# Kernel tuning notes

Hardware: AMD Instinct MI355X
Metric: run time of the kernel (lower is better)

## Reference

```python
import jax, jax.numpy as jnp
import numpy as np

VERTS = [5023, 1256, 314, 79, 20]
SPIRAL_LEN = 9
T_FRAMES = 32
LATENT = 64


def _spiral_conv(x, idx, W, b):
    # x: [B, N, C]; idx: [N, L]; gather spiral neighborhoods then linear
    B = x.shape[0]
    g = x[:, idx.reshape(-1), :].reshape(B, idx.shape[0], -1)  # [B, N, L*C]
    return g @ W.T + b


def _pool(x, rows, cols, vals, n_out):
    # sparse matmul: out[b, rows] += x[b, cols] * vals  (index_select + scatter_add)
    gathered = x[:, cols, :] * vals[None, :, None]
    return jnp.zeros((x.shape[0], n_out, x.shape[2]), x.dtype).at[:, rows, :].add(gathered)


def _lstm_dir(x, Wih, Whh, bih, bhh, reverse):
    # x: [T, B, D]; PyTorch gate order i, f, g, o
    Bz, H = x.shape[1], Whh.shape[1]
    bias = bih + bhh
    def step(carry, xt):
        h, c = carry
        g = xt @ Wih.T + h @ Whh.T + bias
        i, f, gg, o = jnp.split(g, 4, axis=-1)
        c = jax.nn.sigmoid(f) * c + jax.nn.sigmoid(i) * jnp.tanh(gg)
        h = jax.nn.sigmoid(o) * jnp.tanh(c)
        return (h, c), h
    init = (jnp.zeros((Bz, H), x.dtype), jnp.zeros((Bz, H), x.dtype))
    _, hs = jax.lax.scan(step, init, x, reverse=reverse)
    return hs


def _forward(audio_hidden, vertices, actor,
             sp_idx0, sp_idx1, sp_idx2, sp_idx3,
             d0_rows, d0_cols, d0_vals, d1_rows, d1_cols, d1_vals,
             d2_rows, d2_cols, d2_vals, d3_rows, d3_cols, d3_vals,
             u0_rows, u0_cols, u0_vals, u1_rows, u1_cols, u1_vals,
             u2_rows, u2_cols, u2_vals, u3_rows, u3_cols, u3_vals,
             enc_W0, enc_b0, enc_W1, enc_b1, enc_W2, enc_b2, enc_W3, enc_b3,
             enc_lin_W, enc_lin_b, dec_lin_W, dec_lin_b,
             dec_W0, dec_b0, dec_W1, dec_b1, dec_W2, dec_b2, dec_W3, dec_b3,
             dec_W4, dec_b4, aud_W, aud_b,
             l0_Wih, l0_Whh, l0_bih, l0_bhh, l12_Wih, l12_Whh, l12_bih, l12_bhh):
    ah = audio_hidden
    if ah.shape[1] % 2 != 0:
        ah = ah[:, :ah.shape[1] - 1]
    tv = vertices.shape[1]
    if ah.shape[1] > 2 * tv:
        ah = ah[:, :2 * tv]
    elif ah.shape[1] < 2 * tv:
        tv = ah.shape[1] // 2
    hs = ah.reshape(1, ah.shape[1] // 2, ah.shape[2] * 2)[:, :tv]  # [1, T, 1536]
    audio_emb = hs @ aud_W.T + aud_b                                # [1, T, LATENT]
    # --- mesh encoder on actor template: (spiral conv -> ELU -> down pool) x4 -> Linear ---
    sp = (sp_idx0, sp_idx1, sp_idx2, sp_idx3)
    down = ((d0_rows, d0_cols, d0_vals), (d1_rows, d1_cols, d1_vals),
            (d2_rows, d2_cols, d2_vals), (d3_rows, d3_cols, d3_vals))
    encp = ((enc_W0, enc_b0), (enc_W1, enc_b1), (enc_W2, enc_b2), (enc_W3, enc_b3))
    x = actor
    for i in range(4):
        x = jax.nn.elu(_spiral_conv(x, sp[i], *encp[i]))
        x = _pool(x, *down[i], VERTS[i + 1])
    z = x.reshape(x.shape[0], -1) @ enc_lin_W.T + enc_lin_b        # [1, LATENT]
    actor_emb = jnp.broadcast_to(z[:, None, :], audio_emb.shape)
    # --- 3-layer bidirectional LSTM ---
    h = jnp.concatenate([audio_emb, actor_emb], axis=-1).transpose(1, 0, 2)  # [T, 1, 2*LATENT]
    for layer in range(3):
        if layer == 0:
            Wih, Whh, bih, bhh = l0_Wih, l0_Whh, l0_bih, l0_bhh
        else:
            Wih, Whh, bih, bhh = l12_Wih[layer - 1], l12_Whh[layer - 1], l12_bih[layer - 1], l12_bhh[layer - 1]
        f = _lstm_dir(h, Wih[0], Whh[0], bih[0], bhh[0], False)
        r = _lstm_dir(h, Wih[1], Whh[1], bih[1], bhh[1], True)
        h = jnp.concatenate([f, r], axis=-1)
    latent = h.transpose(1, 0, 2)[0]                               # [T, LATENT]
    # --- mesh decoder, batched over all frames (replaces the python per-frame loop) ---
    up = ((u0_rows, u0_cols, u0_vals), (u1_rows, u1_cols, u1_vals),
          (u2_rows, u2_cols, u2_vals), (u3_rows, u3_cols, u3_vals))
    decp = ((dec_W0, dec_b0), (dec_W1, dec_b1), (dec_W2, dec_b2), (dec_W3, dec_b3))
    y = latent @ dec_lin_W.T + dec_lin_b                           # [T, 20*256]
    y = y.reshape(y.shape[0], VERTS[4], -1)                        # [T, 20, 256]
    for i in range(4):
        j = 3 - i
        y = _pool(y, *up[j], VERTS[j])
        y = jax.nn.elu(_spiral_conv(y, sp[j], *decp[i]))
    y = _spiral_conv(y, sp[0], dec_W4, dec_b4)                     # [T, 5023, 3]
    return y + actor                                               # broadcast residual, == vstacked preds


def setup_inputs() -> dict:
    key = jax.random.key(0)
    ks = iter(jax.random.split(key, 96))
    def nrm(shape, s=0.05):
        return jax.random.normal(next(ks), shape, jnp.float32) * s
    def rint(shape, hi):
        return jax.random.randint(next(ks), shape, 0, hi)
    inp = {}
    inp['audio_hidden'] = nrm((1, 2 * T_FRAMES, 768), 1.0)
    inp['vertices'] = nrm((1, T_FRAMES, VERTS[0], 3), 1.0)
    inp['actor'] = nrm((1, VERTS[0], 3), 1.0)
    for i in range(4):
        inp['sp_idx%d' % i] = rint((VERTS[i], SPIRAL_LEN), VERTS[i])
    for i in range(4):
        nnz = 3 * VERTS[i + 1]
        inp['d%d_rows' % i] = rint((nnz,), VERTS[i + 1])
        inp['d%d_cols' % i] = rint((nnz,), VERTS[i])
        inp['d%d_vals' % i] = jax.random.uniform(next(ks), (nnz,), jnp.float32)
    for i in range(4):
        nnz = 3 * VERTS[i]
        inp['u%d_rows' % i] = rint((nnz,), VERTS[i])
        inp['u%d_cols' % i] = rint((nnz,), VERTS[i + 1])
        inp['u%d_vals' % i] = jax.random.uniform(next(ks), (nnz,), jnp.float32)
    OC = [32, 64, 128, 256]
    ic = 3
    for i in range(4):
        inp['enc_W%d' % i] = nrm((OC[i], ic * SPIRAL_LEN))
        inp['enc_b%d' % i] = nrm((OC[i],))
        ic = OC[i]
    inp['enc_lin_W'] = nrm((LATENT, VERTS[4] * OC[3]))
    inp['enc_lin_b'] = nrm((LATENT,))
    inp['dec_lin_W'] = nrm((VERTS[4] * OC[3], LATENT))
    inp['dec_lin_b'] = nrm((VERTS[4] * OC[3],))
    dic = [256, 256, 128, 64]
    doc = [256, 128, 64, 32]
    for i in range(4):
        inp['dec_W%d' % i] = nrm((doc[i], dic[i] * SPIRAL_LEN))
        inp['dec_b%d' % i] = nrm((doc[i],))
    inp['dec_W4'] = nrm((3, OC[0] * SPIRAL_LEN))
    inp['dec_b4'] = nrm((3,))
    inp['aud_W'] = nrm((LATENT, 1536))
    inp['aud_b'] = nrm((LATENT,))
    H = LATENT // 2
    inp['l0_Wih'] = nrm((2, 4 * H, 2 * LATENT))
    inp['l0_Whh'] = nrm((2, 4 * H, H))
    inp['l0_bih'] = nrm((2, 4 * H))
    inp['l0_bhh'] = nrm((2, 4 * H))
    inp['l12_Wih'] = nrm((2, 2, 4 * H, 2 * H))
    inp['l12_Whh'] = nrm((2, 2, 4 * H, H))
    inp['l12_bih'] = nrm((2, 2, 4 * H))
    inp['l12_bhh'] = nrm((2, 2, 4 * H))
    return inp


def reference(audio_hidden, vertices, actor,
              sp_idx0, sp_idx1, sp_idx2, sp_idx3,
              d0_rows, d0_cols, d0_vals, d1_rows, d1_cols, d1_vals,
              d2_rows, d2_cols, d2_vals, d3_rows, d3_cols, d3_vals,
              u0_rows, u0_cols, u0_vals, u1_rows, u1_cols, u1_vals,
              u2_rows, u2_cols, u2_vals, u3_rows, u3_cols, u3_vals,
              enc_W0, enc_b0, enc_W1, enc_b1, enc_W2, enc_b2, enc_W3, enc_b3,
              enc_lin_W, enc_lin_b, dec_lin_W, dec_lin_b,
              dec_W0, dec_b0, dec_W1, dec_b1, dec_W2, dec_b2, dec_W3, dec_b3,
              dec_W4, dec_b4, aud_W, aud_b,
              l0_Wih, l0_Whh, l0_bih, l0_bhh, l12_Wih, l12_Whh, l12_bih, l12_bhh):
    return _forward(audio_hidden, vertices, actor,
                    sp_idx0, sp_idx1, sp_idx2, sp_idx3,
                    d0_rows, d0_cols, d0_vals, d1_rows, d1_cols, d1_vals,
                    d2_rows, d2_cols, d2_vals, d3_rows, d3_cols, d3_vals,
                    u0_rows, u0_cols, u0_vals, u1_rows, u1_cols, u1_vals,
                    u2_rows, u2_cols, u2_vals, u3_rows, u3_cols, u3_vals,
                    enc_W0, enc_b0, enc_W1, enc_b1, enc_W2, enc_b2, enc_W3, enc_b3,
                    enc_lin_W, enc_lin_b, dec_lin_W, dec_lin_b,
                    dec_W0, dec_b0, dec_W1, dec_b1, dec_W2, dec_b2, dec_W3, dec_b3,
                    dec_W4, dec_b4, aud_W, aud_b,
                    l0_Wih, l0_Whh, l0_bih, l0_bhh, l12_Wih, l12_Whh, l12_bih, l12_bhh)
```

## Files before the change

### kernel.cpp

```cpp
#include <hip/hip_runtime.h>
#include <cstdint>
#include <cstddef>


typedef unsigned short u16;
typedef __attribute__((ext_vector_type(8))) short short8;
typedef __attribute__((ext_vector_type(4))) float float4v;
#define CDIV(a,b) (((a)+(b)-1)/(b))
#define POOL_CAP 64

__device__ __forceinline__ float bf(u16 u){ return __uint_as_float(((unsigned)u)<<16); }
__device__ __forceinline__ u16 fb(float x){
  unsigned u = __float_as_uint(x);
  unsigned r = u + 0x7fffu + ((u>>16)&1u);
  return (u16)(r>>16);
}
__device__ __forceinline__ float lo16(unsigned u){ return __uint_as_float(u<<16); }
__device__ __forceinline__ float hi16(unsigned u){ return __uint_as_float(u & 0xffff0000u); }

struct WCast { const float* src[7]; int cum[8]; };
struct Lists {
  const int* rows[8];
  int nnz[8];
  int curoff[8];
  int lstoff[8];
};

__global__ void __launch_bounds__(256) setup_k(
    Lists L, int totN, int NF, int* __restrict__ curBase, int* __restrict__ lstBase,
    WCast C, int totW, int NC, u16* __restrict__ Wbf,
    const float* __restrict__ audio, const float* __restrict__ audW,
    const float* __restrict__ audB, float* __restrict__ h0,
    const float* __restrict__ actor, const int* __restrict__ sp0,
    const float* __restrict__ encW0, const float* __restrict__ encB0,
    u16* __restrict__ outA){
  int blk = blockIdx.x;
  int tid = threadIdx.x;
  if (blk < NF){
    int i = blk*256 + tid;
    if (i < totN){
      int off = i, k = 0;
      while (off >= L.nnz[k]){ off -= L.nnz[k]; k++; }
      int r = L.rows[k][off];
      int p = atomicAdd(curBase + L.curoff[k] + r, 1);
      if (p < POOL_CAP) lstBase[L.lstoff[k] + r*POOL_CAP + p] = off;
    }
    return;
  }
  blk -= NF;
  if (blk < NC){
    int i = blk*256 + tid;
    if (i < totW){
      int k = 0;
      while (i >= C.cum[k+1]) k++;
      Wbf[i] = fb(C.src[k][i - C.cum[k]]);
    }
    return;
  }
  blk -= NC;
  if (blk < 32){
    int t = blk;
    int f = tid >> 2, sl = tid & 3;
    const float4* x4 = (const float4*)(audio + t*1536);
    const float4* w4 = (const float4*)(audW + f*1536);
    float acc = 0.f;
    for (int k=sl; k<384; k+=4){
      float4 xv = x4[k], wv = w4[k];
      acc += xv.x*wv.x + xv.y*wv.y + xv.z*wv.z + xv.w*wv.w;
    }
    acc += __shfl_down(acc, 2, 64);
    acc += __shfl_down(acc, 1, 64);
    if (sl == 0) h0[t*128 + f] = acc + audB[f];
    return;
  }
  blk -= 32;
  int i = blk*256 + tid;
  if (i >= 5023*32) return;
  int o = i % 32; int v = i / 32;
  const float* wrow = encW0 + (size_t)o*27;
  const int* vix = sp0 + v*9;
  float acc = encB0[o];
  for (int s=0;s<9;s++){
    const float* xr = actor + (size_t)vix[s]*3;
    acc += xr[0]*wrow[s*3] + xr[1]*wrow[s*3+1] + xr[2]*wrow[s*3+2];
  }
  if (acc < 0.f) acc = expm1f(acc);
  outA[i] = fb(acc);
}

template<int IC, int BN, int BM>
__global__ void __launch_bounds__(256) conv_mfma(
    const u16* __restrict__ x, const int* __restrict__ idx,
    const u16* __restrict__ Wb, const float* __restrict__ bias,
    u16* __restrict__ out, int V, int OC, int M){
  constexpr int K = 9*IC;
  constexpr int KC = K/32;
  constexpr int NT = BN/16;
  constexpr int MT = BM/64;
  constexpr int LOG2 = (IC==32?5: IC==64?6: IC==128?7:8);
  constexpr int AST = 40;
  __shared__ u16 Asm[2][BM*AST];
  __shared__ u16 Bsm[2][BN*AST];
  __shared__ int rowB[BM], rowV[BM];
  __shared__ int sidx[BM*9];
  int t = threadIdx.x;
  int m0 = blockIdx.x*BM;
  int o0 = blockIdx.y*BN;
  if (t < BM){
    int mg = m0 + t;
    if (mg < M){ int b = mg / V; rowB[t] = b; rowV[t] = mg - b*V; }
    else rowB[t] = -1;
  }
  __syncthreads();
  for (int i=t; i<BM*9; i+=256){
    int r = i/9, s = i - r*9;
    sidx[i] = (rowB[r] >= 0) ? idx[rowV[r]*9 + s] : 0;
  }
  int lane = t & 63, wave = t >> 6;
  int quad = lane >> 4, col = lane & 15;
  float4v acc[MT][NT];
  #pragma unroll
  for (int mi=0;mi<MT;mi++)
    #pragma unroll
    for (int nt=0;nt<NT;nt++) acc[mi][nt] = (float4v)0.f;

  uint4 aval[MT]; uint4 bval;
  auto fetch = [&](int kc){
    int s  = (kc*32) >> LOG2;
    int c0 = (kc*32) & (IC-1);
    #pragma unroll
    for (int rpt=0; rpt<MT; ++rpt){
      int seg = t + 256*rpt;
      int arow = seg >> 2, aq = seg & 3;
      int b = rowB[arow];
      uint4 v = {0u,0u,0u,0u};
      if (b >= 0){
        int ix = sidx[arow*9 + s];
        v = *(const uint4*)(x + ((size_t)b*V + ix)*IC + c0 + aq*8);
      }
      aval[rpt] = v;
    }
    if (t < BN*4){
      int br = t >> 2, bq = t & 3;
      bval = *(const uint4*)(Wb + (size_t)(o0+br)*K + kc*32 + bq*8);
    }
  };

  __syncthreads();
  fetch(0);

  for (int kc = 0; kc < KC; ++kc){
    int buf = kc & 1;
    #pragma unroll
    for (int rpt=0; rpt<MT; ++rpt){
      int seg = t + 256*rpt;
      int arow = seg >> 2, aq = seg & 3;
      *(uint4*)&Asm[buf][arow*AST + aq*8] = aval[rpt];
    }
    if (t < BN*4){
      int br = t >> 2, bq = t & 3;
      *(uint4*)&Bsm[buf][br*AST + bq*8] = bval;
    }
    __syncthreads();
    if (kc+1 < KC) fetch(kc+1);
    short8 a[MT];
    #pragma unroll
    for (int mi=0;mi<MT;mi++)
      a[mi] = *(const short8*)&Asm[buf][(wave*MT*16 + mi*16 + col)*AST + quad*8];
    #pragma unroll
    for (int nt=0; nt<NT; ++nt){
      short8 bfr = *(const short8*)&Bsm[buf][(nt*16 + col)*AST + quad*8];
      #pragma unroll
      for (int mi=0;mi<MT;mi++)
        acc[mi][nt] = __builtin_amdgcn_mfma_f32_16x16x32_bf16(a[mi], bfr, acc[mi][nt], 0, 0, 0);
    }
  }
  #pragma unroll
  for (int mi=0;mi<MT;mi++){
    #pragma unroll
    for (int nt=0; nt<NT; ++nt){
      int o = o0 + nt*16 + col;
      float bv = bias[o];
      #pragma unroll
      for (int r=0;r<4;r++){
        int mg = m0 + wave*MT*16 + mi*16 + quad*4 + r;
        if (mg < M){
          float val = acc[mi][nt][r] + bv;
          if (val < 0.f) val = expm1f(val);
          out[(size_t)mg*OC + o] = fb(val);
        }
      }
    }
  }
}

__global__ void pool_g8_k(const u16* __restrict__ x, const int* __restrict__ cols,
                          const float* __restrict__ vals, const int* __restrict__ cur,
                          const int* __restrict__ lst, u16* __restrict__ out,
                          int B, int Vin, int Vout, int C){
  int C8 = C >> 3;
  int total = B*Vout*C8;
  int i = blockIdx.x*blockDim.x + threadIdx.x;
  if (i >= total) return;
  int c8 = i % C8; int tt = i / C8; int r = tt % Vout; int b = tt / Vout;
  int deg = cur[r]; if (deg > POOL_CAP) deg = POOL_CAP;
  const int* le = lst + r*POOL_CAP;
  float a0=0.f,a1=0.f,a2=0.f,a3=0.f,a4=0.f,a5=0.f,a6=0.f,a7=0.f;
  for (int k=0;k<deg;k++){
    int e = le[k];
    float v = vals[e];
    uint4 xv = *(const uint4*)(x + ((size_t)b*Vin + (size_t)cols[e])*C + c8*8);
    a0 += v*lo16(xv.x); a1 += v*hi16(xv.x);
    a2 += v*lo16(xv.y); a3 += v*hi16(xv.y);
    a4 += v*lo16(xv.z); a5 += v*hi16(xv.z);
    a6 += v*lo16(xv.w); a7 += v*hi16(xv.w);
  }
  uint4 o;
  o.x = ((unsigned)fb(a0)) | (((unsigned)fb(a1))<<16);
  o.y = ((unsigned)fb(a2)) | (((unsigned)fb(a3))<<16);
  o.z = ((unsigned)fb(a4)) | (((unsigned)fb(a5))<<16);
  o.w = ((unsigned)fb(a6)) | (((unsigned)fb(a7))<<16);
  *(uint4*)(out + ((size_t)b*Vout + (size_t)r)*C + c8*8) = o;
}

__global__ void __launch_bounds__(256) enc_lin_k(
    const u16* __restrict__ x, const float* __restrict__ W,
    const float* __restrict__ b, float* __restrict__ h0){
  int f = blockIdx.x;
  int t = threadIdx.x;
  const ushort4* x4 = (const ushort4*)x;
  const float4* w4 = (const float4*)(W + (size_t)f*5120);
  float acc = 0.f;
  for (int k=t; k<1280; k+=256){
    ushort4 xv = x4[k]; float4 wv = w4[k];
    acc += bf(xv.x)*wv.x + bf(xv.y)*wv.y + bf(xv.z)*wv.z + bf(xv.w)*wv.w;
  }
  #pragma unroll
  for (int off=32; off; off>>=1) acc += __shfl_down(acc, off, 64);
  __shared__ float red[4];
  if ((t & 63) == 0) red[t>>6] = acc;
  __syncthreads();
  if (t < 32){
    float zf = b[f] + red[0] + red[1] + red[2] + red[3];
    h0[t*128 + 64 + f] = zf;
  }
}

__device__ __forceinline__ float sigm(float x){ return 1.f/(1.f+__expf(-x)); }
__device__ __forceinline__ float tanhfast(float x){ return 1.f - 2.f/(__expf(2.f*x)+1.f); }

__global__ void __launch_bounds__(256) lstm3_k(
    const float* __restrict__ h0,
    const float* __restrict__ l0_Wih, const float* __restrict__ l0_Whh,
    const float* __restrict__ l0_bih, const float* __restrict__ l0_bhh,
    const float* __restrict__ l12_Wih, const float* __restrict__ l12_Whh,
    const float* __restrict__ l12_bih, const float* __restrict__ l12_bhh,
    float* __restrict__ latent){
  __shared__ __align__(16) u16 xb[32*136];
  __shared__ __align__(16) float xp[2*32*128];
  __shared__ __align__(16) u16 obuf[32*64];
  __shared__ __align__(16) float hsh32[2][32];
  __shared__ float bias_l[256];
  int t = threadIdx.x;
  int lane = t & 63, wave = t >> 6;
  int quad = lane >> 4, col = lane & 15;

  for (int i=t;i<32*128;i+=256){ int tt=i>>7, k=i&127; xb[tt*136+k]=fb(h0[i]); }

  for (int layer=0; layer<3; layer++){
    int IN = (layer==0)?128:64;
    const float *Wih,*Whh,*bih,*bhh;
    if (layer==0){ Wih=l0_Wih; Whh=l0_Whh; bih=l0_bih; bhh=l0_bhh; }
    else {
      int mb=(layer-1)*2;
      Wih=l12_Wih + (size_t)mb*128*64; Whh=l12_Whh + (size_t)mb*128*32;
      bih=l12_bih + mb*128; bhh=l12_bhh + mb*128;
    }
    bias_l[t] = bih[(t>>7)*128 + (t&127)] + bhh[(t>>7)*128 + (t&127)];
    __syncthreads();

    {
      int dirA = wave >> 1, o0 = (wave & 1)*64;
      const float* WA = Wih + (size_t)dirA*128*IN;
      float4v acc[2][4];
      #pragma unroll
      for (int mi=0;mi<2;mi++)
        #pragma unroll
        for (int nt=0;nt<4;nt++) acc[mi][nt] = (float4v)0.f;
      for (int kc=0; kc<IN/32; ++kc){
        short8 bfrag[4];
        #pragma unroll
        for (int nt=0;nt<4;nt++){
          const float* src = WA + (size_t)(o0+nt*16+col)*IN + kc*32 + quad*8;
          float4 w0 = *(const float4*)src;
          float4 w1 = *(const float4*)(src+4);
          alignas(16) u16 tmp[8] = {fb(w0.x),fb(w0.y),fb(w0.z),fb(w0.w),
                                    fb(w1.x),fb(w1.y),fb(w1.z),fb(w1.w)};
          bfrag[nt] = *(const short8*)tmp;
        }
        short8 afrag[2];
        #pragma unroll
        for (int mi=0;mi<2;mi++)
          afrag[mi] = *(const short8*)&xb[(mi*16+col)*136 + kc*32 + quad*8];
        #pragma unroll
        for (int nt=0;nt<4;nt++)
          #pragma unroll
          for (int mi=0;mi<2;mi++)
            acc[mi][nt] = __builtin_amdgcn_mfma_f32_16x16x32_bf16(afrag[mi], bfrag[nt], acc[mi][nt], 0, 0, 0);
      }
      #pragma unroll
      for (int mi=0;mi<2;mi++)
        #pragma unroll
        for (int nt=0;nt<4;nt++){
          int j = o0 + nt*16 + col;
          float bv = bias_l[dirA*128 + j];
          #pragma unroll
          for (int r=0;r<4;r++){
            int tt = mi*16 + quad*4 + r;
            xp[dirA*4096 + tt*128 + j] = acc[mi][nt][r] + bv;
          }
        }
    }
    __syncthreads();

    if (wave < 2){
      int dir = wave; bool rev = (dir == 1);
      int unit = lane & 31, gh = lane >> 5;
      int jA = gh*32 + unit;
      int jB = (gh+2)*32 + unit;
      const float* WD = Whh + (size_t)dir*128*32;
      float wA[32], wB[32];
      #pragma unroll
      for (int k=0;k<32;k++){ wA[k]=WD[(size_t)jA*32+k]; wB[k]=WD[(size_t)jB*32+k]; }
      float* hsd = &hsh32[dir][0];
      if (gh==0) hsd[unit] = 0.f;
      float creg = 0.f;
      const float* xpd = xp + dir*4096;
      float gAc = xpd[(rev?31:0)*128 + jA];
      float gBc = xpd[(rev?31:0)*128 + jB];
      #pragma unroll 1
      for (int s=0;s<32;s++){
        int tx = rev ? (31-s) : s;
        int sn = (s+1 < 32) ? s+1 : 31;
        int txn = rev ? (31-sn) : sn;
        float gA2 = xpd[txn*128 + jA];
        float gB2 = xpd[txn*128 + jB];
        const float4* h4 = (const float4*)hsd;
        float a0=0.f,a1=0.f,a2=0.f,a3=0.f,b0=0.f,b1=0.f,b2=0.f,b3=0.f;
        #pragma unroll
        for (int k=0;k<8;k++){
          float4 hv = h4[k];
          a0=fmaf(hv.x,wA[4*k+0],a0); b0=fmaf(hv.x,wB[4*k+0],b0);
          a1=fmaf(hv.y,wA[4*k+1],a1); b1=fmaf(hv.y,wB[4*k+1],b1);
          a2=fmaf(hv.z,wA[4*k+2],a2); b2=fmaf(hv.z,wB[4*k+2],b2);
          a3=fmaf(hv.w,wA[4*k+3],a3); b3=fmaf(hv.w,wB[4*k+3],b3);
        }
        float gA = gAc + ((a0+a1)+(a2+a3));
        float gB = gBc + ((b0+b1)+(b2+b3));
        float actA = sigm(gA);
        float tB = sigm(gh ? gB : 2.f*gB);
        float actB = gh ? tB : (2.f*tB - 1.f);
        float pA = __shfl_xor(actA, 32, 64);
        float pB = __shfl_xor(actB, 32, 64);
        float gi = gh ? pA : actA;
        float gf = gh ? actA : pA;
        float gg = gh ? pB : actB;
        float go = gh ? actB : pB;
        float cn = fmaf(gf, creg, gi*gg);
        float hn = go * tanhfast(cn);
        creg = cn;
        if (gh==0){
          hsd[unit] = hn;
          obuf[tx*64 + dir*32 + unit] = fb(hn);
        }
        gAc = gA2; gBc = gB2;
      }
    }
    __syncthreads();
    if (layer < 2){
      for (int i=t;i<32*64;i+=256){ int tt=i>>6, k=i&63; xb[tt*136+k]=obuf[i]; }
      __syncthreads();
    }
  }
  for (int i=t;i<32*64;i+=256) latent[i] = bf(obuf[i]);
}

__global__ void dec_lin_k(const float* __restrict__ latent, const float* __restrict__ W,
                          const float* __restrict__ b, u16* __restrict__ y){
  int i = blockIdx.x*blockDim.x + threadIdx.x;
  if (i >= 32*5120) return;
  int r = i % 5120, t = i / 5120;
  const float4* x4 = (const float4*)(latent + t*64);
  const float4* w4 = (const float4*)(W + (size_t)r*64);
  float acc = b[r];
  #pragma unroll
  for (int k=0;k<16;k++){
    float4 xv=x4[k]; float4 wv=w4[k];
    acc += xv.x*wv.x+xv.y*wv.y+xv.z*wv.z+xv.w*wv.w;
  }
  y[i] = fb(acc);
}

__global__ void final_k(const u16* __restrict__ x, const int* __restrict__ idx,
                        const float* __restrict__ W, const float* __restrict__ bias,
                        const float* __restrict__ actor, float* __restrict__ out){
  __shared__ float Wsm[3*288];
  __shared__ float bsm[3];
  int t = threadIdx.x;
  for (int i=t;i<864;i+=256) Wsm[i]=W[i];
  if (t<3) bsm[t]=bias[t];
  __syncthreads();
  int g = blockIdx.x*256 + t;
  if (g >= 32*5023) return;
  int v = g % 5023, b = g / 5023;
  const u16* xb = x + (size_t)b*5023*32;
  const int* vix = idx + v*9;
  float a0=bsm[0], a1=bsm[1], a2=bsm[2];
  for (int s=0;s<9;s++){
    const ushort4* xr = (const ushort4*)(xb + (size_t)vix[s]*32);
    #pragma unroll
    for (int k=0;k<8;k++){
      ushort4 xv = xr[k];
      float x0=bf(xv.x), x1=bf(xv.y), x2=bf(xv.z), x3=bf(xv.w);
      int kk = s*32 + k*4;
      a0 += x0*Wsm[kk] + x1*Wsm[kk+1] + x2*Wsm[kk+2] + x3*Wsm[kk+3];
      a1 += x0*Wsm[288+kk] + x1*Wsm[288+kk+1] + x2*Wsm[288+kk+2] + x3*Wsm[288+kk+3];
      a2 += x0*Wsm[576+kk] + x1*Wsm[576+kk+1] + x2*Wsm[576+kk+2] + x3*Wsm[576+kk+3];
    }
  }
  out[(size_t)g*3+0] = a0 + actor[v*3+0];
  out[(size_t)g*3+1] = a1 + actor[v*3+1];
  out[(size_t)g*3+2] = a2 + actor[v*3+2];
}

extern "C" void kernel_launch(void* const* d_in, const int* in_sizes, int n_in,
                              void* d_out, int out_size, void* d_ws, size_t ws_size,
                              hipStream_t stream){
  (void)in_sizes; (void)n_in; (void)out_size; (void)ws_size;

  const float* audio = (const float*)d_in[0];
  const float* actor = (const float*)d_in[2];
  const int* sp[4]   = {(const int*)d_in[3],(const int*)d_in[4],(const int*)d_in[5],(const int*)d_in[6]};
  const int* drows[4]; const int* dcols[4]; const float* dvals[4];
  for (int i=0;i<4;i++){ drows[i]=(const int*)d_in[7+3*i]; dcols[i]=(const int*)d_in[8+3*i]; dvals[i]=(const float*)d_in[9+3*i]; }
  const int* urows[4]; const int* ucols[4]; const float* uvals[4];
  for (int i=0;i<4;i++){ urows[i]=(const int*)d_in[19+3*i]; ucols[i]=(const int*)d_in[20+3*i]; uvals[i]=(const float*)d_in[21+3*i]; }
  const float* encW[4]={(const float*)d_in[31],(const float*)d_in[33],(const float*)d_in[35],(const float*)d_in[37]};
  const float* encB[4]={(const float*)d_in[32],(const float*)d_in[34],(const float*)d_in[36],(const float*)d_in[38]};
  const float* enc_lin_W=(const float*)d_in[39]; const float* enc_lin_b=(const float*)d_in[40];
  const float* dec_lin_W=(const float*)d_in[41]; const float* dec_lin_b=(const float*)d_in[42];
  const float* decW[5]={(const float*)d_in[43],(const float*)d_in[45],(const float*)d_in[47],(const float*)d_in[49],(const float*)d_in[51]};
  const float* decB[5]={(const float*)d_in[44],(const float*)d_in[46],(const float*)d_in[48],(const float*)d_in[50],(const float*)d_in[52]};
  const float* audW=(const float*)d_in[53]; const float* audB=(const float*)d_in[54];
  const float* l0_Wih=(const float*)d_in[55]; const float* l0_Whh=(const float*)d_in[56];
  const float* l0_bih=(const float*)d_in[57]; const float* l0_bhh=(const float*)d_in[58];
  const float* l12_Wih=(const float*)d_in[59]; const float* l12_Whh=(const float*)d_in[60];
  const float* l12_bih=(const float*)d_in[61]; const float* l12_bhh=(const float*)d_in[62];
  float* out = (float*)d_out;

  char* base = (char*)d_ws;
  u16* A  = (u16*)base;
  u16* Bb = (u16*)(base + 10287104);
  int* curBase = (int*)(base + 30891520);
  int* lstBase = (int*)(base + 30924928);
  u16* Wbf = (u16*)(base + 33060224);
  float* sm = (float*)(base + 35788160);
  float* h0     = sm;
  float* latent = sm + 4096;

  const int wsz[7] = {64*288, 128*576, 256*1152, 256*2304, 128*2304, 64*1152, 32*576};
  WCast WC; int wcum = 0;
  const float* wsrc[7] = {encW[1],encW[2],encW[3],decW[0],decW[1],decW[2],decW[3]};
  int wo[7];
  for (int k=0;k<7;k++){ WC.src[k]=wsrc[k]; WC.cum[k]=wcum; wo[k]=wcum; wcum+=wsz[k]; }
  WC.cum[7]=wcum;

  const int pVout[8] = {1256,314,79,20,5023,1256,314,79};
  const int pNnz[8]  = {3768,942,237,60,15069,3768,942,237};
  Lists L; int curoff=0, lstoff=0, totnnz=0;
  const int* prow[8] = {drows[0],drows[1],drows[2],drows[3],urows[0],urows[1],urows[2],urows[3]};
  int curo[8], lsto[8];
  for (int k=0;k<8;k++){
    L.rows[k]=prow[k]; L.nnz[k]=pNnz[k];
    L.curoff[k]=curoff; L.lstoff[k]=lstoff;
    curo[k]=curoff; lsto[k]=lstoff;
    curoff += pVout[k]; lstoff += pVout[k]*POOL_CAP; totnnz += pNnz[k];
  }
  hipMemsetAsync(curBase, 0, (size_t)curoff*4, stream);

  int NF = CDIV(totnnz,256), NC = CDIV(wcum,256), NC3 = CDIV(5023*32,256);
  setup_k<<<NF+NC+32+NC3,256,0,stream>>>(L, totnnz, NF, curBase, lstBase,
                                         WC, wcum, NC, Wbf,
                                         audio, audW, audB, h0,
                                         actor, sp[0], encW[0], encB[0], A);

  pool_g8_k<<<CDIV(1256*4,256),256,0,stream>>>(A, dcols[0], dvals[0], curBase+curo[0], lstBase+lsto[0], Bb, 1, 5023, 1256, 32);
  conv_mfma<32,64,64><<<dim3(CDIV(1256,64),1),256,0,stream>>>(Bb, sp[1], Wbf+wo[0], encB[1], A, 1256, 64, 1256);
  pool_g8_k<<<CDIV(314*8,256),256,0,stream>>>(A, dcols[1], dvals[1], curBase+curo[1], lstBase+lsto[1], Bb, 1, 1256, 314, 64);
  conv_mfma<64,64,64><<<dim3(CDIV(314,64),2),256,0,stream>>>(Bb, sp[2], Wbf+wo[1], encB[2], A, 314, 128, 314);
  pool_g8_k<<<CDIV(79*16,256),256,0,stream>>>(A, dcols[2], dvals[2], curBase+curo[2], lstBase+lsto[2], Bb, 1, 314, 79, 128);
  conv_mfma<128,64,64><<<dim3(CDIV(79,64),4),256,0,stream>>>(Bb, sp[3], Wbf+wo[2], encB[3], A, 79, 256, 79);
  pool_g8_k<<<CDIV(20*32,256),256,0,stream>>>(A, dcols[3], dvals[3], curBase+curo[3], lstBase+lsto[3], Bb, 1, 79, 20, 256);

  enc_lin_k<<<64,256,0,stream>>>(Bb, enc_lin_W, enc_lin_b, h0);

  lstm3_k<<<1,256,0,stream>>>(h0, l0_Wih, l0_Whh, l0_bih, l0_bhh,
                              l12_Wih, l12_Whh, l12_bih, l12_bhh, latent);

  dec_lin_k<<<CDIV(32*5120,256),256,0,stream>>>(latent, dec_lin_W, dec_lin_b, A);

  pool_g8_k<<<CDIV(32*79*32,256),256,0,stream>>>(A, ucols[3], uvals[3], curBase+curo[7], lstBase+lsto[7], Bb, 32, 20, 79, 256);
  conv_mfma<256,64,64><<<dim3(CDIV(2528,64),4),256,0,stream>>>(Bb, sp[3], Wbf+wo[3], decB[0], A, 79, 256, 2528);

  pool_g8_k<<<CDIV(32*314*32,256),256,0,stream>>>(A, ucols[2], uvals[2], curBase+curo[6], lstBase+lsto[6], Bb, 32, 79, 314, 256);
  conv_mfma<256,64,64><<<dim3(CDIV(10048,64),2),256,0,stream>>>(Bb, sp[2], Wbf+wo[4], decB[1], A, 314, 128, 10048);

  pool_g8_k<<<CDIV(32*1256*16,256),256,0,stream>>>(A, ucols[1], uvals[1], curBase+curo[5], lstBase+lsto[5], Bb, 32, 314, 1256, 128);
  conv_mfma<128,64,128><<<dim3(CDIV(40192,128),1),256,0,stream>>>(Bb, sp[1], Wbf+wo[5], decB[2], A, 1256, 64, 40192);

  pool_g8_k<<<CDIV(32*5023*8,256),256,0,stream>>>(A, ucols[0], uvals[0], curBase+curo[4], lstBase+lsto[4], Bb, 32, 1256, 5023, 64);
  conv_mfma<64,32,128><<<dim3(CDIV(160736,128),1),256,0,stream>>>(Bb, sp[0], Wbf+wo[6], decB[3], A, 5023, 32, 160736);

  final_k<<<CDIV(32*5023,256),256,0,stream>>>(A, sp[0], decW[4], decB[4], actor, out);
}
```

Baseline: 569.2 us.

## Fuse encoder spiral conv with downsample pool into per-output-vertex fp32 stage kernels

Replaces the encoder's separate conv_mfma and pool kernels with a fused fp32 kernel per level. Each kernel computes the spiral conv plus ELU only at the source vertices each pooled output needs, then applies the sparse weights. This drops four launches and the bf16 conversion of the encoder weights. In exchange, convs are recomputed for vertices shared by several outputs, use scalar fp32 dot products instead of MFMA, and each thread reads its own weight row without reuse.

Measured after the change: 961.7 us. 69.0% more time.

```diff
diff --git a/kernel.cpp b/kernel.cpp
--- a/kernel.cpp
+++ b/kernel.cpp
@@ -18,7 +18,7 @@
 __device__ __forceinline__ float lo16(unsigned u){ return __uint_as_float(u<<16); }
 __device__ __forceinline__ float hi16(unsigned u){ return __uint_as_float(u & 0xffff0000u); }
 
-struct WCast { const float* src[7]; int cum[8]; };
+struct WCast { const float* src[4]; int cum[5]; };
 struct Lists {
   const int* rows[8];
   int nnz[8];
@@ -30,10 +30,7 @@
     Lists L, int totN, int NF, int* __restrict__ curBase, int* __restrict__ lstBase,
     WCast C, int totW, int NC, u16* __restrict__ Wbf,
     const float* __restrict__ audio, const float* __restrict__ audW,
-    const float* __restrict__ audB, float* __restrict__ h0,
-    const float* __restrict__ actor, const int* __restrict__ sp0,
-    const float* __restrict__ encW0, const float* __restrict__ encB0,
-    u16* __restrict__ outA){
+    const float* __restrict__ audB, float* __restrict__ h0){
   int blk = blockIdx.x;
   int tid = threadIdx.x;
   if (blk < NF){
@@ -58,34 +55,60 @@
     return;
   }
   blk -= NC;
-  if (blk < 32){
-    int t = blk;
-    int f = tid >> 2, sl = tid & 3;
-    const float4* x4 = (const float4*)(audio + t*1536);
-    const float4* w4 = (const float4*)(audW + f*1536);
-    float acc = 0.f;
-    for (int k=sl; k<384; k+=4){
-      float4 xv = x4[k], wv = w4[k];
-      acc += xv.x*wv.x + xv.y*wv.y + xv.z*wv.z + xv.w*wv.w;
-    }
-    acc += __shfl_down(acc, 2, 64);
-    acc += __shfl_down(acc, 1, 64);
-    if (sl == 0) h0[t*128 + f] = acc + audB[f];
-    return;
-  }
-  blk -= 32;
-  int i = blk*256 + tid;
-  if (i >= 5023*32) return;
-  int o = i % 32; int v = i / 32;
-  const float* wrow = encW0 + (size_t)o*27;
-  const int* vix = sp0 + v*9;
-  float acc = encB0[o];
-  for (int s=0;s<9;s++){
-    const float* xr = actor + (size_t)vix[s]*3;
-    acc += xr[0]*wrow[s*3] + xr[1]*wrow[s*3+1] + xr[2]*wrow[s*3+2];
-  }
-  if (acc < 0.f) acc = expm1f(acc);
-  outA[i] = fb(acc);
+  int t = blk;
+  int f = tid >> 2, sl = tid & 3;
+  const float4* x4 = (const float4*)(audio + t*1536);
+  const float4* w4 = (const float4*)(audW + f*1536);
+  float acc = 0.f;
+  for (int k=sl; k<384; k+=4){
+    float4 xv = x4[k], wv = w4[k];
+    acc += xv.x*wv.x + xv.y*wv.y + xv.z*wv.z + xv.w*wv.w;
+  }
+  acc += __shfl_down(acc, 2, 64);
+  acc += __shfl_down(acc, 1, 64);
+  if (sl == 0) h0[t*128 + f] = acc + audB[f];
+}
+
+template<int IC, int OC>
+__global__ void __launch_bounds__(256) fstage_k(
+    const float* __restrict__ x, const int* __restrict__ sp,
+    const int* __restrict__ cols, const float* __restrict__ vals,
+    const int* __restrict__ cur, const int* __restrict__ lst,
+    const float* __restrict__ W, const float* __restrict__ bias,
+    float* __restrict__ out, int Vout){
+  int i = blockIdx.x*256 + threadIdx.x;
+  if (i >= Vout*OC) return;
+  int c = i % OC, r = i / OC;
+  int deg = cur[r]; if (deg > POOL_CAP) deg = POOL_CAP;
+  const int* le = lst + r*POOL_CAP;
+  float bc = bias[c];
+  const float* wc = W + (size_t)c*9*IC;
+  float acc = 0.f;
+  for (int k=0;k<deg;k++){
+    int e = le[k];
+    float v = vals[e];
+    const int* vix = sp + cols[e]*9;
+    float s = bc;
+    #pragma unroll
+    for (int j=0;j<9;j++){
+      const float* xr = x + (size_t)vix[j]*IC;
+      const float* wr = wc + j*IC;
+      if constexpr (IC % 4 == 0){
+        #pragma unroll 4
+        for (int k2=0;k2<IC;k2+=4){
+          float4 xv = *(const float4*)(xr+k2);
+          float4 wv = *(const float4*)(wr+k2);
+          s += xv.x*wv.x + xv.y*wv.y + xv.z*wv.z + xv.w*wv.w;
+        }
+      } else {
+        #pragma unroll
+        for (int k2=0;k2<IC;k2++) s += xr[k2]*wr[k2];
+      }
+    }
+    if (s < 0.f) s = expm1f(s);
+    acc += v*s;
+  }
+  out[(size_t)r*OC + c] = acc;
 }
 
 template<int IC, int BN, int BM>
@@ -224,16 +247,16 @@
 }
 
 __global__ void __launch_bounds__(256) enc_lin_k(
-    const u16* __restrict__ x, const float* __restrict__ W,
+    const float* __restrict__ x, const float* __restrict__ W,
     const float* __restrict__ b, float* __restrict__ h0){
   int f = blockIdx.x;
   int t = threadIdx.x;
-  const ushort4* x4 = (const ushort4*)x;
+  const float4* x4 = (const float4*)x;
   const float4* w4 = (const float4*)(W + (size_t)f*5120);
   float acc = 0.f;
   for (int k=t; k<1280; k+=256){
-    ushort4 xv = x4[k]; float4 wv = w4[k];
-    acc += bf(xv.x)*wv.x + bf(xv.y)*wv.y + bf(xv.z)*wv.z + bf(xv.w)*wv.w;
+    float4 xv = x4[k]; float4 wv = w4[k];
+    acc += xv.x*wv.x + xv.y*wv.y + xv.z*wv.z + xv.w*wv.w;
   }
   #pragma unroll
   for (int off=32; off; off>>=1) acc += __shfl_down(acc, off, 64);
@@ -468,12 +491,17 @@
   float* h0     = sm;
   float* latent = sm + 4096;
 
-  const int wsz[7] = {64*288, 128*576, 256*1152, 256*2304, 128*2304, 64*1152, 32*576};
+  float* xe1 = (float*)Bb;
+  float* xe2 = xe1 + 40192;
+  float* xe3 = xe2 + 20096;
+  float* xe4 = xe3 + 10112;
+
+  const int wsz[4] = {256*2304, 128*2304, 64*1152, 32*576};
   WCast WC; int wcum = 0;
-  const float* wsrc[7] = {encW[1],encW[2],encW[3],decW[0],decW[1],decW[2],decW[3]};
-  int wo[7];
-  for (int k=0;k<7;k++){ WC.src[k]=wsrc[k]; WC.cum[k]=wcum; wo[k]=wcum; wcum+=wsz[k]; }
-  WC.cum[7]=wcum;
+  const float* wsrc[4] = {decW[0],decW[1],decW[2],decW[3]};
+  int wo[4];
+  for (int k=0;k<4;k++){ WC.src[k]=wsrc[k]; WC.cum[k]=wcum; wo[k]=wcum; wcum+=wsz[k]; }
+  WC.cum[4]=wcum;
 
   const int pVout[8] = {1256,314,79,20,5023,1256,314,79};
   const int pNnz[8]  = {3768,942,237,60,15069,3768,942,237};
@@ -488,21 +516,25 @@
   }
   hipMemsetAsync(curBase, 0, (size_t)curoff*4, stream);
 
-  int NF = CDIV(totnnz,256), NC = CDIV(wcum,256), NC3 = CDIV(5023*32,256);
-  setup_k<<<NF+NC+32+NC3,256,0,stream>>>(L, totnnz, NF, curBase, lstBase,
-                                         WC, wcum, NC, Wbf,
-                                         audio, audW, audB, h0,
-                                         actor, sp[0], encW[0], encB[0], A);
-
-  pool_g8_k<<<CDIV(1256*4,256),256,0,stream>>>(A, dcols[0], dvals[0], curBase+curo[0], lstBase+lsto[0], Bb, 1, 5023, 1256, 32);
-  conv_mfma<32,64,64><<<dim3(CDIV(1256,64),1),256,0,stream>>>(Bb, sp[1], Wbf+wo[0], encB[1], A, 1256, 64, 1256);
-  pool_g8_k<<<CDIV(314*8,256),256,0,stream>>>(A, dcols[1], dvals[1], curBase+curo[1], lstBase+lsto[1], Bb, 1, 1256, 314, 64);
-  conv_mfma<64,64,64><<<dim3(CDIV(314,64),2),256,0,stream>>>(Bb, sp[2], Wbf+wo[1], encB[2], A, 314, 128, 314);
-  pool_g8_k<<<CDIV(79*16,256),256,0,stream>>>(A, dcols[2], dvals[2], curBase+curo[2], lstBase+lsto[2], Bb, 1, 314, 79, 128);
-  conv_mfma<128,64,64><<<dim3(CDIV(79,64),4),256,0,stream>>>(Bb, sp[3], Wbf+wo[2], encB[3], A, 79, 256, 79);
-  pool_g8_k<<<CDIV(20*32,256),256,0,stream>>>(A, dcols[3], dvals[3], curBase+curo[3], lstBase+lsto[3], Bb, 1, 79, 20, 256);
-
-  enc_lin_k<<<64,256,0,stream>>>(Bb, enc_lin_W, enc_lin_b, h0);
+  int NF = CDIV(totnnz,256), NC = CDIV(wcum,256);
+  setup_k<<<NF+NC+32,256,0,stream>>>(L, totnnz, NF, curBase, lstBase,
+                                     WC, wcum, NC, Wbf,
+                                     audio, audW, audB, h0);
+
+  fstage_k<3,32><<<CDIV(1256*32,256),256,0,stream>>>(
+      actor, sp[0], dcols[0], dvals[0], curBase+curo[0], lstBase+lsto[0],
+      encW[0], encB[0], xe1, 1256);
+  fstage_k<32,64><<<CDIV(314*64,256),256,0,stream>>>(
+      xe1, sp[1], dcols[1], dvals[1], curBase+curo[1], lstBase+lsto[1],
+      encW[1], encB[1], xe2, 314);
+  fstage_k<64,128><<<CDIV(79*128,256),256,0,stream>>>(
+      xe2, sp[2], dcols[2], dvals[2], curBase+curo[2], lstBase+lsto[2],
+      encW[2], encB[2], xe3, 79);
+  fstage_k<128,256><<<CDIV(20*256,256),256,0,stream>>>(
+      xe3, sp[3], dcols[3], dvals[3], curBase+curo[3], lstBase+lsto[3],
+      encW[3], encB[3], xe4, 20);
+
+  enc_lin_k<<<64,256,0,stream>>>(xe4, enc_lin_W, enc_lin_b, h0);
 
   lstm3_k<<<1,256,0,stream>>>(h0, l0_Wih, l0_Whh, l0_bih, l0_bhh,
                               l12_Wih, l12_Whh, l12_bih, l12_bhh, latent);
@@ -510,16 +542,16 @@
   dec_lin_k<<<CDIV(32*5120,256),256,0,stream>>>(latent, dec_lin_W, dec_lin_b, A);
 
   pool_g8_k<<<CDIV(32*79*32,256),256,0,stream>>>(A, ucols[3], uvals[3], curBase+curo[7], lstBase+lsto[7], Bb, 32, 20, 79, 256);
-  conv_mfma<256,64,64><<<dim3(CDIV(2528,64),4),256,0,stream>>>(Bb, sp[3], Wbf+wo[3], decB[0], A, 79, 256, 2528);
+  conv_mfma<256,64,64><<<dim3(CDIV(2528,64),4),256,0,stream>>>(Bb, sp[3], Wbf+wo[0], decB[0], A, 79, 256, 2528);
 
   pool_g8_k<<<CDIV(32*314*32,256),256,0,stream>>>(A, ucols[2], uvals[2], curBase+curo[6], lstBase+lsto[6], Bb, 32, 79, 314, 256);
-  conv_mfma<256,64,64><<<dim3(CDIV(10048,64),2),256,0,stream>>>(Bb, sp[2], Wbf+wo[4], decB[1], A, 314, 128, 10048);
+  conv_mfma<256,64,64><<<dim3(CDIV(10048,64),2),256,0,stream>>>(Bb, sp[2], Wbf+wo[1], decB[1], A, 314, 128, 10048);
 
   pool_g8_k<<<CDIV(32*1256*16,256),256,0,stream>>>(A, ucols[1], uvals[1], curBase+curo[5], lstBase+lsto[5], Bb, 32, 314, 1256, 128);
-  conv_mfma<128,64,128><<<dim3(CDIV(40192,128),1),256,0,stream>>>(Bb, sp[1], Wbf+wo[5], decB[2], A, 1256, 64, 40192);
+  conv_mfma<128,64,128><<<dim3(CDIV(40192,128),1),256,0,stream>>>(Bb, sp[1], Wbf+wo[2], decB[2], A, 1256, 64, 40192);
 
   pool_g8_k<<<CDIV(32*5023*8,256),256,0,stream>>>(A, ucols[0], uvals[0], curBase+curo[4], lstBase+lsto[4], Bb, 32, 1256, 5023, 64);
-  conv_mfma<64,32,128><<<dim3(CDIV(160736,128),1),256,0,stream>>>(Bb, sp[0], Wbf+wo[6], decB[3], A, 5023, 32, 160736);
+  conv_mfma<64,32,128><<<dim3(CDIV(160736,128),1),256,0,stream>>>(Bb, sp[0], Wbf+wo[3], decB[3], A, 5023, 32, 160736);
 
   final_k<<<CDIV(32*5023,256),256,0,stream>>>(A, sp[0], decW[4], decB[4], actor, out);
 }
```

## Fuse first conv into down-pool, fold dec linear into up-pool matrix

Applied to the files above, without the earlier changes.

The first spiral conv is now computed inside the first down-pool kernel, only at the vertices the pool actually reads, so the full-resolution intermediate is never written. The last down-pool is merged with the encoder linear layer in one single-block kernel. The decoder linear layer and the first up-pool are folded algebraically: setup_k builds a combined matrix and bias from the pool weights and dec_lin on every call, and one kernel then applies them to the latent. This removes several launches and intermediate round trips to memory. In exchange the setup pass gains brute-force scans over the pool entries, and the decoder step does more multiply-adds per output.

Measured after the change: 676.4 us. +18.8%, slower.

```diff
diff --git a/kernel.cpp b/kernel.cpp
--- a/kernel.cpp
+++ b/kernel.cpp
@@ -31,9 +31,10 @@
     WCast C, int totW, int NC, u16* __restrict__ Wbf,
     const float* __restrict__ audio, const float* __restrict__ audW,
     const float* __restrict__ audB, float* __restrict__ h0,
-    const float* __restrict__ actor, const int* __restrict__ sp0,
-    const float* __restrict__ encW0, const float* __restrict__ encB0,
-    u16* __restrict__ outA){
+    const int* __restrict__ u3rows, const int* __restrict__ u3cols,
+    const float* __restrict__ u3vals,
+    const float* __restrict__ dlW, const float* __restrict__ dlb,
+    float* __restrict__ M, float* __restrict__ bp, int NM){
   int blk = blockIdx.x;
   int tid = threadIdx.x;
   if (blk < NF){
@@ -74,18 +75,60 @@
     return;
   }
   blk -= 32;
+  if (blk < NM){
+    int i = blk*256 + tid;
+    if (i >= 79*256*16) return;
+    int k4 = i & 15; int rc = i >> 4;
+    int c = rc & 255; int r = rc >> 8;
+    float4 acc = {0.f,0.f,0.f,0.f};
+    for (int e=0; e<237; ++e){
+      if (u3rows[e] == r){
+        float v = u3vals[e];
+        float4 w = *(const float4*)(dlW + ((size_t)(u3cols[e]*256 + c))*64 + k4*4);
+        acc.x += v*w.x; acc.y += v*w.y; acc.z += v*w.z; acc.w += v*w.w;
+      }
+    }
+    *(float4*)(M + (size_t)rc*64 + k4*4) = acc;
+    return;
+  }
+  blk -= NM;
   int i = blk*256 + tid;
-  if (i >= 5023*32) return;
-  int o = i % 32; int v = i / 32;
-  const float* wrow = encW0 + (size_t)o*27;
-  const int* vix = sp0 + v*9;
-  float acc = encB0[o];
-  for (int s=0;s<9;s++){
-    const float* xr = actor + (size_t)vix[s]*3;
-    acc += xr[0]*wrow[s*3] + xr[1]*wrow[s*3+1] + xr[2]*wrow[s*3+2];
-  }
-  if (acc < 0.f) acc = expm1f(acc);
-  outA[i] = fb(acc);
+  if (i >= 79*256) return;
+  int c = i & 255; int r = i >> 8;
+  float acc = 0.f;
+  for (int e=0; e<237; ++e)
+    if (u3rows[e] == r) acc += u3vals[e]*dlb[u3cols[e]*256 + c];
+  bp[i] = acc;
+}
+
+__global__ void __launch_bounds__(256) fs1_k(
+    const float* __restrict__ x, const int* __restrict__ sp,
+    const int* __restrict__ cols, const float* __restrict__ vals,
+    const int* __restrict__ cur, const int* __restrict__ lst,
+    const float* __restrict__ W, const float* __restrict__ bias,
+    u16* __restrict__ out){
+  int i = blockIdx.x*256 + threadIdx.x;
+  if (i >= 1256*32) return;
+  int c = i & 31, r = i >> 5;
+  int deg = cur[r]; if (deg > POOL_CAP) deg = POOL_CAP;
+  const int* le = lst + r*POOL_CAP;
+  float bc = bias[c];
+  const float* wc = W + (size_t)c*27;
+  float acc = 0.f;
+  for (int k=0;k<deg;k++){
+    int e = le[k];
+    float v = vals[e];
+    const int* vix = sp + cols[e]*9;
+    float s = bc;
+    #pragma unroll
+    for (int j=0;j<9;j++){
+      const float* xr = x + (size_t)vix[j]*3;
+      s += xr[0]*wc[j*3] + xr[1]*wc[j*3+1] + xr[2]*wc[j*3+2];
+    }
+    if (s < 0.f) s = expm1f(s);
+    acc += v*s;
+  }
+  out[i] = fb(acc);
 }
 
 template<int IC, int BN, int BM>
@@ -223,26 +266,39 @@
   *(uint4*)(out + ((size_t)b*Vout + (size_t)r)*C + c8*8) = o;
 }
 
-__global__ void __launch_bounds__(256) enc_lin_k(
-    const u16* __restrict__ x, const float* __restrict__ W,
+__global__ void __launch_bounds__(256) pd3enclin_k(
+    const u16* __restrict__ x, const int* __restrict__ cols,
+    const float* __restrict__ vals, const int* __restrict__ cur,
+    const int* __restrict__ lst, const float* __restrict__ W,
     const float* __restrict__ b, float* __restrict__ h0){
-  int f = blockIdx.x;
+  __shared__ __align__(16) float xl[5120];
   int t = threadIdx.x;
-  const ushort4* x4 = (const ushort4*)x;
+  for (int i=t; i<5120; i+=256){
+    int r = i >> 8, c = i & 255;
+    int deg = cur[r]; if (deg > POOL_CAP) deg = POOL_CAP;
+    const int* le = lst + r*POOL_CAP;
+    float acc = 0.f;
+    for (int k=0;k<deg;k++){
+      int e = le[k];
+      acc += vals[e]*bf(x[(size_t)cols[e]*256 + c]);
+    }
+    xl[i] = acc;
+  }
+  __syncthreads();
+  int f = t >> 2, sl = t & 3;
   const float4* w4 = (const float4*)(W + (size_t)f*5120);
+  const float4* x4 = (const float4*)xl;
   float acc = 0.f;
-  for (int k=t; k<1280; k+=256){
-    ushort4 xv = x4[k]; float4 wv = w4[k];
-    acc += bf(xv.x)*wv.x + bf(xv.y)*wv.y + bf(xv.z)*wv.z + bf(xv.w)*wv.w;
-  }
-  #pragma unroll
-  for (int off=32; off; off>>=1) acc += __shfl_down(acc, off, 64);
-  __shared__ float red[4];
-  if ((t & 63) == 0) red[t>>6] = acc;
-  __syncthreads();
-  if (t < 32){
-    float zf = b[f] + red[0] + red[1] + red[2] + red[3];
-    h0[t*128 + 64 + f] = zf;
+  for (int k=sl; k<1280; k+=4){
+    float4 xv = x4[k], wv = w4[k];
+    acc += xv.x*wv.x + xv.y*wv.y + xv.z*wv.z + xv.w*wv.w;
+  }
+  acc += __shfl_down(acc, 2, 64);
+  acc += __shfl_down(acc, 1, 64);
+  if (sl == 0){
+    float zf = b[f] + acc;
+    #pragma unroll
+    for (int tt=0; tt<32; ++tt) h0[tt*128 + 64 + f] = zf;
   }
 }
 
@@ -385,20 +441,22 @@
   for (int i=t;i<32*64;i+=256) latent[i] = bf(obuf[i]);
 }
 
-__global__ void dec_lin_k(const float* __restrict__ latent, const float* __restrict__ W,
-                          const float* __restrict__ b, u16* __restrict__ y){
-  int i = blockIdx.x*blockDim.x + threadIdx.x;
-  if (i >= 32*5120) return;
-  int r = i % 5120, t = i / 5120;
+__global__ void __launch_bounds__(256) dlp_k(
+    const float* __restrict__ latent, const float* __restrict__ M,
+    const float* __restrict__ bp, u16* __restrict__ y){
+  int i = blockIdx.x*256 + threadIdx.x;
+  if (i >= 32*79*256) return;
+  int c = i & 255; int rt = i >> 8;
+  int r = rt % 79; int t = rt / 79;
+  const float4* m4 = (const float4*)(M + ((size_t)r*256 + c)*64);
   const float4* x4 = (const float4*)(latent + t*64);
-  const float4* w4 = (const float4*)(W + (size_t)r*64);
-  float acc = b[r];
+  float acc = bp[r*256 + c];
   #pragma unroll
   for (int k=0;k<16;k++){
-    float4 xv=x4[k]; float4 wv=w4[k];
-    acc += xv.x*wv.x+xv.y*wv.y+xv.z*wv.z+xv.w*wv.w;
-  }
-  y[i] = fb(acc);
+    float4 xv = x4[k], mv = m4[k];
+    acc += xv.x*mv.x + xv.y*mv.y + xv.z*mv.z + xv.w*mv.w;
+  }
+  y[((size_t)t*79 + r)*256 + c] = fb(acc);
 }
 
 __global__ void final_k(const u16* __restrict__ x, const int* __restrict__ idx,
@@ -467,6 +525,8 @@
   float* sm = (float*)(base + 35788160);
   float* h0     = sm;
   float* latent = sm + 4096;
+  float* Mf = (float*)(base + 4194304);
+  float* bp = (float*)(base + 9437184);
 
   const int wsz[7] = {64*288, 128*576, 256*1152, 256*2304, 128*2304, 64*1152, 32*576};
   WCast WC; int wcum = 0;
@@ -488,28 +548,29 @@
   }
   hipMemsetAsync(curBase, 0, (size_t)curoff*4, stream);
 
-  int NF = CDIV(totnnz,256), NC = CDIV(wcum,256), NC3 = CDIV(5023*32,256);
-  setup_k<<<NF+NC+32+NC3,256,0,stream>>>(L, totnnz, NF, curBase, lstBase,
-                                         WC, wcum, NC, Wbf,
-                                         audio, audW, audB, h0,
-                                         actor, sp[0], encW[0], encB[0], A);
-
-  pool_g8_k<<<CDIV(1256*4,256),256,0,stream>>>(A, dcols[0], dvals[0], curBase+curo[0], lstBase+lsto[0], Bb, 1, 5023, 1256, 32);
+  int NF = CDIV(totnnz,256), NC = CDIV(wcum,256);
+  int NM = CDIV(79*256*16,256), NB = CDIV(79*256,256);
+  setup_k<<<NF+NC+32+NM+NB,256,0,stream>>>(L, totnnz, NF, curBase, lstBase,
+                                           WC, wcum, NC, Wbf,
+                                           audio, audW, audB, h0,
+                                           urows[3], ucols[3], uvals[3],
+                                           dec_lin_W, dec_lin_b, Mf, bp, NM);
+
+  fs1_k<<<CDIV(1256*32,256),256,0,stream>>>(
+      actor, sp[0], dcols[0], dvals[0], curBase+curo[0], lstBase+lsto[0],
+      encW[0], encB[0], Bb);
   conv_mfma<32,64,64><<<dim3(CDIV(1256,64),1),256,0,stream>>>(Bb, sp[1], Wbf+wo[0], encB[1], A, 1256, 64, 1256);
   pool_g8_k<<<CDIV(314*8,256),256,0,stream>>>(A, dcols[1], dvals[1], curBase+curo[1], lstBase+lsto[1], Bb, 1, 1256, 314, 64);
   conv_mfma<64,64,64><<<dim3(CDIV(314,64),2),256,0,stream>>>(Bb, sp[2], Wbf+wo[1], encB[2], A, 314, 128, 314);
   pool_g8_k<<<CDIV(79*16,256),256,0,stream>>>(A, dcols[2], dvals[2], curBase+curo[2], lstBase+lsto[2], Bb, 1, 314, 79, 128);
   conv_mfma<128,64,64><<<dim3(CDIV(79,64),4),256,0,stream>>>(Bb, sp[3], Wbf+wo[2], encB[3], A, 79, 256, 79);
-  pool_g8_k<<<CDIV(20*32,256),256,0,stream>>>(A, dcols[3], dvals[3], curBase+curo[3], lstBase+lsto[3], Bb, 1, 79, 20, 256);
-
-  enc_lin_k<<<64,256,0,stream>>>(Bb, enc_lin_W, enc_lin_b, h0);
+  pd3enclin_k<<<1,256,0,stream>>>(A, dcols[3], dvals[3], curBase+curo[3], lstBase+lsto[3],
+                                  enc_lin_W, enc_lin_b, h0);
 
   lstm3_k<<<1,256,0,stream>>>(h0, l0_Wih, l0_Whh, l0_bih, l0_bhh,
                               l12_Wih, l12_Whh, l12_bih, l12_bhh, latent);
 
-  dec_lin_k<<<CDIV(32*5120,256),256,0,stream>>>(latent, dec_lin_W, dec_lin_b, A);
-
-  pool_g8_k<<<CDIV(32*79*32,256),256,0,stream>>>(A, ucols[3], uvals[3], curBase+curo[7], lstBase+lsto[7], Bb, 32, 20, 79, 256);
+  dlp_k<<<CDIV(32*79*256,256),256,0,stream>>>(latent, Mf, bp, Bb);
   conv_mfma<256,64,64><<<dim3(CDIV(2528,64),4),256,0,stream>>>(Bb, sp[3], Wbf+wo[3], decB[0], A, 79, 256, 2528);
 
   pool_g8_k<<<CDIV(32*314*32,256),256,0,stream>>>(A, ucols[2], uvals[2], curBase+curo[6], lstBase+lsto[6], Bb, 32, 79, 314, 256);
```
